# Kernel tuning notes

Hardware: AMD Instinct MI355X
Metric: run time of the kernel (lower is better)

## Reference

```python
import jax, jax.numpy as jnp
import numpy as np
import math

N_HEAD = 32
HEAD_DIM = 64
ROTARY_DIM = 32
ROTARY_BASE = 10000.0
NEG_INF = -10000.0


def _rope_cos_sin(seqlen):
    # RotaryEmbedding._update_cos_sin_cache: inv_freq over even indices of rotary_dim
    inv_freq = 1.0 / (ROTARY_BASE ** (jnp.arange(0, ROTARY_DIM, 2, dtype=jnp.float32) / ROTARY_DIM))
    t = jnp.arange(seqlen, dtype=jnp.float32)
    freqs = jnp.outer(t, inv_freq)  # [s, rd/2]
    return jnp.cos(freqs), jnp.sin(freqs)


def _apply_rotary(t, cos, sin):
    # t: [b, s, h, d]; GPT-NeoX half-rotation on first ROTARY_DIM dims, pass-through rest
    half = ROTARY_DIM // 2
    x1 = t[..., :half]
    x2 = t[..., half:ROTARY_DIM]
    x_pass = t[..., ROTARY_DIM:]
    c = cos[:, None, :]  # [s, 1, rd/2] -> broadcasts over (b, s, h, rd/2)
    s_ = sin[:, None, :]
    return jnp.concatenate([x1 * c - x2 * s_, x1 * s_ + x2 * c, x_pass], axis=-1)


def setup_inputs() -> dict:
    key = jax.random.key(0)
    k1, k2, k3, k4, k5 = jax.random.split(key, 5)
    b, s, e = 2, 2048, 2048
    return {
        "x": jax.random.normal(k1, (b, s, e), dtype=jnp.float32),
        "Wqkv": jax.random.normal(k2, (e, 3 * e), dtype=jnp.float32) * 0.02,
        "bqkv": jax.random.normal(k3, (3 * e,), dtype=jnp.float32) * 0.02,
        "Wout": jax.random.normal(k4, (e, e), dtype=jnp.float32) * 0.02,
        "bout": jax.random.normal(k5, (e,), dtype=jnp.float32) * 0.02,
    }


def reference(x, Wqkv, bqkv, Wout, bout):
    b, s, e = x.shape
    # QKV projection -> [b, s, 3, h, d]
    qkv = (x @ Wqkv + bqkv).reshape(b, s, 3, N_HEAD, HEAD_DIM)
    cos, sin = _rope_cos_sin(s)
    q = _apply_rotary(qkv[:, :, 0], cos, sin)
    k = _apply_rotary(qkv[:, :, 1], cos, sin)
    v = qkv[:, :, 2]
    # Attention (SelfAttention/CrossAttention math, fp32, materialized scores)
    scale = 1.0 / math.sqrt(HEAD_DIM)
    scores = jnp.einsum('bthd,bshd->bhts', q, k * scale)  # [b, h, s, s]
    rows = jnp.arange(s)[:, None]
    cols = jnp.arange(s)[None, :]
    causal_mask = cols > rows  # seqlen_q == seqlen_k
    scores = jnp.where(causal_mask, NEG_INF, scores)
    attn = jax.nn.softmax(scores, axis=-1)
    out = jnp.einsum('bhts,bshd->bthd', attn, v).reshape(b, s, e)
    return out @ Wout + bout
```

## Files before the change

kernel.cpp:

```cpp
#include <hip/hip_runtime.h>


typedef _Float16 half8 __attribute__((ext_vector_type(8)));
typedef _Float16 half4 __attribute__((ext_vector_type(4)));
typedef float floatx4 __attribute__((ext_vector_type(4)));

#define GLD_LDS16(gp, sp)                                        \
  __builtin_amdgcn_global_load_lds(                              \
      (__attribute__((address_space(1))) void*)(gp),             \
      (__attribute__((address_space(3))) void*)(sp), 16, 0, 0)

__device__ __forceinline__ floatx4 mfma16(half8 a, half8 b, floatx4 c) {
  return __builtin_amdgcn_mfma_f32_16x16x32_f16(a, b, c, 0, 0, 0);
}
__device__ __forceinline__ floatx4 mfma16k16(half4 a, half4 b, floatx4 c) {
  return __builtin_amdgcn_mfma_f32_16x16x16f16(a, b, c, 0, 0, 0);
}

__global__ __launch_bounds__(256) void cvt_x_kernel(const float* __restrict__ x,
                                                    _Float16* __restrict__ xh) {
  int idx = blockIdx.x * 256 + threadIdx.x;
  const floatx4* p = (const floatx4*)x + (size_t)idx * 2;
  floatx4 a = p[0], b = p[1];
  half8 o;
#pragma unroll
  for (int j = 0; j < 4; ++j) { o[j] = (_Float16)a[j]; o[4 + j] = (_Float16)b[j]; }
  *((half8*)xh + idx) = o;
}

__global__ __launch_bounds__(256) void cvt_wt_kernel(const float* __restrict__ W,
                                                     _Float16* __restrict__ Wt,
                                                     int Kd, int Nd) {
  __shared__ float tile[64][65];
  int n0 = blockIdx.x * 64, k0 = blockIdx.y * 64;
  int tid = threadIdx.x;
#pragma unroll
  for (int it = 0; it < 4; ++it) {
    int r = (tid >> 4) + it * 16;
    int c = (tid & 15) * 4;
    floatx4 v = *(const floatx4*)(W + (size_t)(k0 + r) * Nd + n0 + c);
    tile[r][c + 0] = v[0]; tile[r][c + 1] = v[1];
    tile[r][c + 2] = v[2]; tile[r][c + 3] = v[3];
  }
  __syncthreads();
#pragma unroll
  for (int it = 0; it < 2; ++it) {
    int r = (tid >> 3) + it * 32;
    int c = (tid & 7) * 8;
    half8 o;
#pragma unroll
    for (int j = 0; j < 8; ++j) o[j] = (_Float16)tile[c + j][r];
    *(half8*)(Wt + (size_t)(n0 + r) * Kd + k0 + c) = o;
  }
}

__global__ __launch_bounds__(512, 2) void gemm_qkv_kernel(
    const _Float16* __restrict__ A, const _Float16* __restrict__ Bt,
    const float* __restrict__ bias,
    _Float16* __restrict__ Qd, _Float16* __restrict__ Kkd,
    _Float16* __restrict__ Vd) {
  __shared__ __align__(16) _Float16 sA[2][16384];
  __shared__ __align__(16) _Float16 sB[2][12288];
  constexpr int KD = 2048;
  constexpr int NT = KD / 64;

  int tid = threadIdx.x, w = tid >> 6, l = tid & 63;
  int lr = l & 15, quad = l >> 4;
  int wr = w >> 1, wc = w & 1;
  int m0 = blockIdx.y * 256, n0 = blockIdx.x * 192;

  int csw0 = ((quad) ^ (lr & 7)) * 8;
  int csw1 = ((quad + 4) ^ (lr & 7)) * 8;

  const _Float16* pA[4];
  const _Float16* pB[3];
  {
    int rl = l >> 3;
    int cs = ((l & 7) ^ rl) * 8;
#pragma unroll
    for (int jj = 0; jj < 4; ++jj)
      pA[jj] = A + (size_t)(m0 + w * 32 + jj * 8 + rl) * KD + cs;
#pragma unroll
    for (int jj = 0; jj < 3; ++jj)
      pB[jj] = Bt + (size_t)(n0 + w * 24 + jj * 8 + rl) * KD + cs;
  }

#define STAGE_ALL(BUF, KT)                                                   \
  _Pragma("unroll") for (int jj = 0; jj < 4; ++jj)                           \
    GLD_LDS16(pA[jj] + (KT), &sA[BUF][(w * 32 + jj * 8) * 64]);              \
  _Pragma("unroll") for (int jj = 0; jj < 3; ++jj)                           \
    GLD_LDS16(pB[jj] + (KT), &sB[BUF][(w * 24 + jj * 8) * 64]);

  floatx4 z4 = {0.f, 0.f, 0.f, 0.f};
  floatx4 acc[4][6];
#pragma unroll
  for (int i = 0; i < 4; ++i)
#pragma unroll
    for (int j = 0; j < 6; ++j) acc[i][j] = z4;

  STAGE_ALL(0, 0);
  asm volatile("s_waitcnt vmcnt(0)" ::: "memory");
  __builtin_amdgcn_s_barrier();

  half8 af[4][2], bf[6][2];
#pragma unroll 2
  for (int t = 0; t < NT; ++t) {
    int buf = t & 1, nbuf = buf ^ 1;
    if (t + 1 < NT) { STAGE_ALL(nbuf, (t + 1) * 64); }
#pragma unroll
    for (int j = 0; j < 6; ++j) {
      int row_ = wc * 96 + j * 16 + lr;
      bf[j][0] = *(const half8*)&sB[buf][row_ * 64 + csw0];
      bf[j][1] = *(const half8*)&sB[buf][row_ * 64 + csw1];
    }
#pragma unroll
    for (int i = 0; i < 4; ++i) {
      int row_ = wr * 64 + i * 16 + lr;
      af[i][0] = *(const half8*)&sA[buf][row_ * 64 + csw0];
      af[i][1] = *(const half8*)&sA[buf][row_ * 64 + csw1];
    }
    __builtin_amdgcn_s_setprio(1);
#pragma unroll
    for (int j = 0; j < 6; ++j)
#pragma unroll
      for (int ks = 0; ks < 2; ++ks)
#pragma unroll
        for (int i = 0; i < 4; ++i)
          acc[i][j] = mfma16(af[i][ks], bf[j][ks], acc[i][j]);
    __builtin_amdgcn_s_setprio(0);
    asm volatile("s_waitcnt vmcnt(0)" ::: "memory");
    __builtin_amdgcn_s_barrier();
  }

  float bj[6];
#pragma unroll
  for (int j = 0; j < 6; ++j) bj[j] = bias[n0 + wc * 96 + j * 16 + lr];
  float freq = __expf(-(float)lr * 0.57564627324851148f);
#pragma unroll
  for (int j = 0; j < 6; ++j) {
    int cb = wc * 96 + j * 16;
    int cg = n0 + cb;
    int which = cg >> 11;
    int d0 = cb & 63;
    int hh = (cg & 2047) >> 6;
    if (which == 2) {
      int dd = d0 + lr;
#pragma unroll
      for (int i = 0; i < 4; ++i) {
        int m = m0 + wr * 64 + i * 16 + quad * 4;
        int bb = m >> 11, tt = m & 2047;
        half4 h;
#pragma unroll
        for (int r = 0; r < 4; ++r) h[r] = (_Float16)(acc[i][j][r] + bj[j]);
        *(half4*)&Vd[(((size_t)(bb * 32 + hh)) * 64 + dd) * 2048 + tt] = h;
      }
    } else if (d0 == 0) {
      _Float16* dst = which ? Kkd : Qd;
#pragma unroll
      for (int i = 0; i < 4; ++i)
#pragma unroll
        for (int r = 0; r < 4; ++r) {
          int m = m0 + wr * 64 + i * 16 + quad * 4 + r;
          int bb = m >> 11, tt = m & 2047;
          float sn, cs2;
          __sincosf((float)tt * freq, &sn, &cs2);
          float x1 = acc[i][j][r] + bj[j];
          float x2 = acc[i][j + 1][r] + bj[j + 1];
          _Float16* row = dst + ((size_t)(bb * 32 + hh) * 2048 + (size_t)tt) * 64;
          row[lr] = (_Float16)(x1 * cs2 - x2 * sn);
          row[lr + 16] = (_Float16)(x1 * sn + x2 * cs2);
        }
    } else if (d0 >= 32) {
      _Float16* dst = which ? Kkd : Qd;
#pragma unroll
      for (int i = 0; i < 4; ++i)
#pragma unroll
        for (int r = 0; r < 4; ++r) {
          int m = m0 + wr * 64 + i * 16 + quad * 4 + r;
          int bb = m >> 11, tt = m & 2047;
          _Float16* row = dst + ((size_t)(bb * 32 + hh) * 2048 + (size_t)tt) * 64;
          row[d0 + lr] = (_Float16)(acc[i][j][r] + bj[j]);
        }
    }
  }
#undef STAGE_ALL
}

__global__ __launch_bounds__(512, 2) void gemm_out_kernel(
    const _Float16* __restrict__ A, const _Float16* __restrict__ Bt,
    const float* __restrict__ bias, float* __restrict__ Co) {
  __shared__ __align__(16) _Float16 sA[2][16384];
  __shared__ __align__(16) _Float16 sB[2][8192];
  constexpr int KD = 2048;
  constexpr int NT = KD / 64;

  int tid = threadIdx.x, w = tid >> 6, l = tid & 63;
  int lr = l & 15, quad = l >> 4;
  int wr = w >> 1, wc = w & 1;
  int m0 = blockIdx.y * 256, n0 = blockIdx.x * 128;

  int csw0 = ((quad) ^ (lr & 7)) * 8;
  int csw1 = ((quad + 4) ^ (lr & 7)) * 8;

  const _Float16* pA[4];
  const _Float16* pB[2];
  {
    int rl = l >> 3;
    int cs = ((l & 7) ^ rl) * 8;
#pragma unroll
    for (int jj = 0; jj < 4; ++jj)
      pA[jj] = A + (size_t)(m0 + w * 32 + jj * 8 + rl) * KD + cs;
#pragma unroll
    for (int jj = 0; jj < 2; ++jj)
      pB[jj] = Bt + (size_t)(n0 + w * 16 + jj * 8 + rl) * KD + cs;
  }

#define STAGE_O(BUF, KT)                                                     \
  _Pragma("unroll") for (int jj = 0; jj < 4; ++jj)                           \
    GLD_LDS16(pA[jj] + (KT), &sA[BUF][(w * 32 + jj * 8) * 64]);              \
  _Pragma("unroll") for (int jj = 0; jj < 2; ++jj)                           \
    GLD_LDS16(pB[jj] + (KT), &sB[BUF][(w * 16 + jj * 8) * 64]);

  floatx4 z4 = {0.f, 0.f, 0.f, 0.f};
  floatx4 acc[4][4];
#pragma unroll
  for (int i = 0; i < 4; ++i)
#pragma unroll
    for (int j = 0; j < 4; ++j) acc[i][j] = z4;

  STAGE_O(0, 0);
  asm volatile("s_waitcnt vmcnt(0)" ::: "memory");
  __builtin_amdgcn_s_barrier();

  half8 af[4][2], bf[4][2];
#pragma unroll 2
  for (int t = 0; t < NT; ++t) {
    int buf = t & 1, nbuf = buf ^ 1;
    if (t + 1 < NT) { STAGE_O(nbuf, (t + 1) * 64); }
#pragma unroll
    for (int j = 0; j < 4; ++j) {
      int row_ = wc * 64 + j * 16 + lr;
      bf[j][0] = *(const half8*)&sB[buf][row_ * 64 + csw0];
      bf[j][1] = *(const half8*)&sB[buf][row_ * 64 + csw1];
    }
#pragma unroll
    for (int i = 0; i < 4; ++i) {
      int row_ = wr * 64 + i * 16 + lr;
      af[i][0] = *(const half8*)&sA[buf][row_ * 64 + csw0];
      af[i][1] = *(const half8*)&sA[buf][row_ * 64 + csw1];
    }
    __builtin_amdgcn_s_setprio(1);
#pragma unroll
    for (int j = 0; j < 4; ++j)
#pragma unroll
      for (int ks = 0; ks < 2; ++ks)
#pragma unroll
        for (int i = 0; i < 4; ++i)
          acc[i][j] = mfma16(af[i][ks], bf[j][ks], acc[i][j]);
    __builtin_amdgcn_s_setprio(0);
    asm volatile("s_waitcnt vmcnt(0)" ::: "memory");
    __builtin_amdgcn_s_barrier();
  }

#pragma unroll
  for (int j = 0; j < 4; ++j) {
    int n = n0 + wc * 64 + j * 16 + lr;
    float bj = bias[n];
#pragma unroll
    for (int i = 0; i < 4; ++i)
#pragma unroll
      for (int r = 0; r < 4; ++r) {
        int m = m0 + wr * 64 + i * 16 + quad * 4 + r;
        Co[(size_t)m * 2048 + n] = acc[i][j][r] + bj;
      }
  }
#undef STAGE_O
}

__global__ __launch_bounds__(256, 4) void attn_kernel(
    const _Float16* __restrict__ Q, const _Float16* __restrict__ Kk,
    const _Float16* __restrict__ Vt, _Float16* __restrict__ O) {
  constexpr int S = 2048;
  int bh = blockIdx.x;
  int qt = 15 - blockIdx.y;
  int bb = bh >> 5, hh = bh & 31;
  const _Float16* Qb = Q + (size_t)bh * S * 64;
  const _Float16* Kb = Kk + (size_t)bh * S * 64;
  const _Float16* Vb = Vt + (size_t)bh * 64 * S;

  __shared__ __align__(16) _Float16 sK[128 * 72];
  __shared__ __align__(16) _Float16 sVt[64 * 136];

  int tid = threadIdx.x, w = tid >> 6, l = tid & 63;
  int lr = l & 15, quad = l >> 4;

  int rk = tid >> 3, ck = (tid & 7) * 8;
  int rv = tid >> 4, cv = (tid & 15) * 8;
  const _Float16* Kst = Kb + (size_t)rk * 64 + ck;
  const _Float16* Vst = Vb + (size_t)rv * S + cv;

  floatx4 z4 = {0.f, 0.f, 0.f, 0.f};
  int q0 = qt * 128;

  half8 qf[2][2];
#pragma unroll
  for (int qtl = 0; qtl < 2; ++qtl)
#pragma unroll
    for (int ks = 0; ks < 2; ++ks) {
      half8 v = *(const half8*)(Qb + (size_t)(q0 + w * 32 + qtl * 16 + lr) * 64 +
                                ks * 32 + quad * 8);
      qf[qtl][ks] = v * (_Float16)0.18033688f;
    }

  floatx4 Oa[4][2];
  float m_i[2] = {-1e30f, -1e30f}, l_i[2] = {0.f, 0.f};
#pragma unroll
  for (int dt = 0; dt < 4; ++dt)
#pragma unroll
    for (int qtl = 0; qtl < 2; ++qtl) Oa[dt][qtl] = z4;

  half8 kpre[4];
#pragma unroll
  for (int it = 0; it < 4; ++it)
    kpre[it] = *(const half8*)(Kst + (size_t)it * 32 * 64);

  for (int jt = 0; jt <= qt; ++jt) {
    half8 vcur[4];
#pragma unroll
    for (int it = 0; it < 4; ++it)
      vcur[it] = *(const half8*)(Vst + (size_t)jt * 128 + (size_t)it * 16 * S);
#pragma unroll
    for (int it = 0; it < 4; ++it)
      *(half8*)&sK[(rk + it * 32) * 72 + ck] = kpre[it];
    if (jt < qt) {
      int kv1 = (jt + 1) * 128;
#pragma unroll
      for (int it = 0; it < 4; ++it)
        kpre[it] = *(const half8*)(Kst + (size_t)(kv1 + it * 32) * 64);
    }
#pragma unroll
    for (int it = 0; it < 4; ++it)
      *(half8*)&sVt[(rv + it * 16) * 136 + cv] = vcur[it];
    __syncthreads();

#pragma unroll
    for (int qtl = 0; qtl < 2; ++qtl) {
      floatx4 Sa[8];
#pragma unroll
      for (int kvt = 0; kvt < 8; ++kvt) Sa[kvt] = z4;
      __builtin_amdgcn_s_setprio(1);
#pragma unroll
      for (int ks = 0; ks < 2; ++ks)
#pragma unroll
        for (int kvt = 0; kvt < 8; ++kvt) {
          half8 kf = *(const half8*)&sK[(kvt * 16 + lr) * 72 + ks * 32 + quad * 8];
          Sa[kvt] = mfma16(kf, qf[qtl][ks], Sa[kvt]);
        }
      __builtin_amdgcn_s_setprio(0);

      if (jt == qt) {
        int q_loc = w * 32 + qtl * 16 + lr;
#pragma unroll
        for (int kvt = 0; kvt < 8; ++kvt) {
          int kv_base = kvt * 16 + quad * 4;
#pragma unroll
          for (int r = 0; r < 4; ++r)
            if (kv_base + r > q_loc) Sa[kvt][r] = -1e30f;
        }
      }

      float mx = Sa[0][0];
#pragma unroll
      for (int kvt = 0; kvt < 8; ++kvt)
#pragma unroll
        for (int r = 0; r < 4; ++r) mx = fmaxf(mx, Sa[kvt][r]);
      mx = fmaxf(mx, __shfl_xor(mx, 16));
      mx = fmaxf(mx, __shfl_xor(mx, 32));
      float mnew = fmaxf(m_i[qtl], mx);
      if (!__all(mx <= m_i[qtl])) {
        float alpha = __builtin_amdgcn_exp2f(m_i[qtl] - mnew);
        l_i[qtl] *= alpha;
#pragma unroll
        for (int dt = 0; dt < 4; ++dt) Oa[dt][qtl] *= alpha;
      }
      m_i[qtl] = mnew;
      float rs = 0.f;
#pragma unroll
      for (int kvt = 0; kvt < 8; ++kvt)
#pragma unroll
        for (int r = 0; r < 4; ++r) {
          float p = __builtin_amdgcn_exp2f(Sa[kvt][r] - mnew);
          Sa[kvt][r] = p;
          rs += p;
        }
      rs += __shfl_xor(rs, 16);
      rs += __shfl_xor(rs, 32);
      l_i[qtl] += rs;

      __builtin_amdgcn_s_setprio(1);
#pragma unroll
      for (int kvt = 0; kvt < 8; ++kvt) {
        half4 vf[4];
#pragma unroll
        for (int dt = 0; dt < 4; ++dt)
          vf[dt] = *(const half4*)&sVt[(dt * 16 + lr) * 136 + kvt * 16 + quad * 4];
        half4 pf;
        pf[0] = (_Float16)Sa[kvt][0];
        pf[1] = (_Float16)Sa[kvt][1];
        pf[2] = (_Float16)Sa[kvt][2];
        pf[3] = (_Float16)Sa[kvt][3];
#pragma unroll
        for (int dt = 0; dt < 4; ++dt)
          Oa[dt][qtl] = mfma16k16(vf[dt], pf, Oa[dt][qtl]);
      }
      __builtin_amdgcn_s_setprio(0);
    }
    __syncthreads();
  }

  float inv0 = 1.0f / l_i[0], inv1 = 1.0f / l_i[1];
#pragma unroll
  for (int dt = 0; dt < 4; ++dt)
#pragma unroll
    for (int qtl = 0; qtl < 2; ++qtl) {
      float inv = qtl ? inv1 : inv0;
      floatx4 o = Oa[dt][qtl];
      half4 hv;
      hv[0] = (_Float16)(o[0] * inv); hv[1] = (_Float16)(o[1] * inv);
      hv[2] = (_Float16)(o[2] * inv); hv[3] = (_Float16)(o[3] * inv);
      *(half4*)&sK[(w * 32 + qtl * 16 + lr) * 72 + dt * 16 + quad * 4] = hv;
    }
  __syncthreads();
#pragma unroll
  for (int it = 0; it < 2; ++it) {
    int row = (tid >> 2) + it * 64;
    int t = q0 + row;
    _Float16* orow = O + ((size_t)(bb * 2048 + t)) * 2048 + hh * 64;
#pragma unroll
    for (int cc = 0; cc < 2; ++cc) {
      int col = (tid & 3) * 16 + cc * 8;
      *(half8*)(orow + col) = *(const half8*)&sK[row * 72 + col];
    }
  }
}

extern "C" void kernel_launch(void* const* d_in, const int* in_sizes, int n_in,
                              void* d_out, int out_size, void* d_ws, size_t ws_size,
                              hipStream_t stream) {
  (void)in_sizes; (void)n_in; (void)out_size; (void)ws_size;
  const float* x = (const float*)d_in[0];
  const float* Wqkv = (const float*)d_in[1];
  const float* bqkv = (const float*)d_in[2];
  const float* Wout = (const float*)d_in[3];
  const float* bout = (const float*)d_in[4];
  float* out = (float*)d_out;
  char* ws = (char*)d_ws;

  _Float16* xh    = (_Float16*)(ws + 0);
  _Float16* wqkvt = (_Float16*)(ws + 16777216);
  _Float16* Oh    = (_Float16*)(ws + 16777216);
  _Float16* Qh    = (_Float16*)(ws + 41943040);
  _Float16* Kh    = (_Float16*)(ws + 58720256);
  _Float16* Vth   = (_Float16*)(ws + 75497472);
  _Float16* woutt = (_Float16*)(ws + 92274688);

  cvt_x_kernel<<<4096, 256, 0, stream>>>(x, xh);
  cvt_wt_kernel<<<dim3(96, 32), 256, 0, stream>>>(Wqkv, wqkvt, 2048, 6144);
  cvt_wt_kernel<<<dim3(32, 32), 256, 0, stream>>>(Wout, woutt, 2048, 2048);
  gemm_qkv_kernel<<<dim3(32, 16), 512, 0, stream>>>(xh, wqkvt, bqkv, Qh, Kh, Vth);
  attn_kernel<<<dim3(64, 16), 256, 0, stream>>>(Qh, Kh, Vth, Oh);
  gemm_out_kernel<<<dim3(16, 16), 512, 0, stream>>>(Oh, woutt, bout, out);
}
```

Measured before the change: 389.8 us.

## Merge conversion kernels, prefetch V tiles, and interleave both query subtiles in attention

Combines the x and weight fp16 conversion kernels into one launch dispatched by block index, removing two kernel launches. In attention, V tiles are now prefetched one iteration ahead into registers, like K, instead of loaded and stored within the same iteration. Both 16-row query subtiles are computed together in the QK and PV MFMA loops, so each K/V fragment read from shared memory feeds two MFMAs. The occupancy hint of 4 blocks is removed from launch_bounds, and together with the extra live registers this may lower occupancy.

Result: no change. 390.8 us (+0.3%).

```diff
diff --git a/kernel.cpp b/kernel.cpp
--- a/kernel.cpp
+++ b/kernel.cpp
@@ -17,23 +17,34 @@
   return __builtin_amdgcn_mfma_f32_16x16x16f16(a, b, c, 0, 0, 0);
 }
 
-__global__ __launch_bounds__(256) void cvt_x_kernel(const float* __restrict__ x,
-                                                    _Float16* __restrict__ xh) {
-  int idx = blockIdx.x * 256 + threadIdx.x;
-  const floatx4* p = (const floatx4*)x + (size_t)idx * 2;
-  floatx4 a = p[0], b = p[1];
-  half8 o;
-#pragma unroll
-  for (int j = 0; j < 4; ++j) { o[j] = (_Float16)a[j]; o[4 + j] = (_Float16)b[j]; }
-  *((half8*)xh + idx) = o;
-}
-
-__global__ __launch_bounds__(256) void cvt_wt_kernel(const float* __restrict__ W,
-                                                     _Float16* __restrict__ Wt,
-                                                     int Kd, int Nd) {
+__global__ __launch_bounds__(256) void cvt_all_kernel(
+    const float* __restrict__ x, _Float16* __restrict__ xh,
+    const float* __restrict__ Wqkv, _Float16* __restrict__ wqkvt,
+    const float* __restrict__ Wout, _Float16* __restrict__ woutt) {
   __shared__ float tile[64][65];
-  int n0 = blockIdx.x * 64, k0 = blockIdx.y * 64;
-  int tid = threadIdx.x;
+  int b = blockIdx.x, tid = threadIdx.x;
+  if (b < 4096) {
+    int idx = b * 256 + tid;
+    const floatx4* p = (const floatx4*)x + (size_t)idx * 2;
+    floatx4 a = p[0], b2 = p[1];
+    half8 o;
+#pragma unroll
+    for (int j = 0; j < 4; ++j) { o[j] = (_Float16)a[j]; o[4 + j] = (_Float16)b2[j]; }
+    *((half8*)xh + idx) = o;
+    return;
+  }
+  const float* W;
+  _Float16* Wt;
+  int Kd, Nd, n0, k0;
+  if (b < 7168) {
+    int bb = b - 4096;
+    W = Wqkv; Wt = wqkvt; Kd = 2048; Nd = 6144;
+    n0 = (bb % 96) * 64; k0 = (bb / 96) * 64;
+  } else {
+    int bb = b - 7168;
+    W = Wout; Wt = woutt; Kd = 2048; Nd = 2048;
+    n0 = (bb % 32) * 64; k0 = (bb / 32) * 64;
+  }
 #pragma unroll
   for (int it = 0; it < 4; ++it) {
     int r = (tid >> 4) + it * 16;
@@ -277,7 +288,7 @@
 #undef STAGE_O
 }
 
-__global__ __launch_bounds__(256, 4) void attn_kernel(
+__global__ __launch_bounds__(256) void attn_kernel(
     const _Float16* __restrict__ Q, const _Float16* __restrict__ Kk,
     const _Float16* __restrict__ Vt, _Float16* __restrict__ O) {
   constexpr int S = 2048;
@@ -319,61 +330,67 @@
 #pragma unroll
     for (int qtl = 0; qtl < 2; ++qtl) Oa[dt][qtl] = z4;
 
-  half8 kpre[4];
-#pragma unroll
-  for (int it = 0; it < 4; ++it)
+  half8 kpre[4], vpre[4];
+#pragma unroll
+  for (int it = 0; it < 4; ++it) {
     kpre[it] = *(const half8*)(Kst + (size_t)it * 32 * 64);
+    vpre[it] = *(const half8*)(Vst + (size_t)it * 16 * S);
+  }
 
   for (int jt = 0; jt <= qt; ++jt) {
-    half8 vcur[4];
-#pragma unroll
-    for (int it = 0; it < 4; ++it)
-      vcur[it] = *(const half8*)(Vst + (size_t)jt * 128 + (size_t)it * 16 * S);
-#pragma unroll
-    for (int it = 0; it < 4; ++it)
+#pragma unroll
+    for (int it = 0; it < 4; ++it) {
       *(half8*)&sK[(rk + it * 32) * 72 + ck] = kpre[it];
+      *(half8*)&sVt[(rv + it * 16) * 136 + cv] = vpre[it];
+    }
     if (jt < qt) {
       int kv1 = (jt + 1) * 128;
 #pragma unroll
-      for (int it = 0; it < 4; ++it)
+      for (int it = 0; it < 4; ++it) {
         kpre[it] = *(const half8*)(Kst + (size_t)(kv1 + it * 32) * 64);
-    }
-#pragma unroll
-    for (int it = 0; it < 4; ++it)
-      *(half8*)&sVt[(rv + it * 16) * 136 + cv] = vcur[it];
+        vpre[it] = *(const half8*)(Vst + kv1 + (size_t)it * 16 * S);
+      }
+    }
     __syncthreads();
 
-#pragma unroll
-    for (int qtl = 0; qtl < 2; ++qtl) {
-      floatx4 Sa[8];
-#pragma unroll
-      for (int kvt = 0; kvt < 8; ++kvt) Sa[kvt] = z4;
-      __builtin_amdgcn_s_setprio(1);
-#pragma unroll
-      for (int ks = 0; ks < 2; ++ks)
-#pragma unroll
-        for (int kvt = 0; kvt < 8; ++kvt) {
-          half8 kf = *(const half8*)&sK[(kvt * 16 + lr) * 72 + ks * 32 + quad * 8];
-          Sa[kvt] = mfma16(kf, qf[qtl][ks], Sa[kvt]);
-        }
-      __builtin_amdgcn_s_setprio(0);
-
-      if (jt == qt) {
+    floatx4 Sa[2][8];
+#pragma unroll
+    for (int qtl = 0; qtl < 2; ++qtl)
+#pragma unroll
+      for (int kvt = 0; kvt < 8; ++kvt) Sa[qtl][kvt] = z4;
+    __builtin_amdgcn_s_setprio(1);
+#pragma unroll
+    for (int ks = 0; ks < 2; ++ks) {
+#pragma unroll
+      for (int kvt = 0; kvt < 8; ++kvt) {
+        half8 kf = *(const half8*)&sK[(kvt * 16 + lr) * 72 + ks * 32 + quad * 8];
+        Sa[0][kvt] = mfma16(kf, qf[0][ks], Sa[0][kvt]);
+        Sa[1][kvt] = mfma16(kf, qf[1][ks], Sa[1][kvt]);
+      }
+    }
+    __builtin_amdgcn_s_setprio(0);
+
+    if (jt == qt) {
+#pragma unroll
+      for (int qtl = 0; qtl < 2; ++qtl) {
         int q_loc = w * 32 + qtl * 16 + lr;
 #pragma unroll
         for (int kvt = 0; kvt < 8; ++kvt) {
           int kv_base = kvt * 16 + quad * 4;
 #pragma unroll
           for (int r = 0; r < 4; ++r)
-            if (kv_base + r > q_loc) Sa[kvt][r] = -1e30f;
+            if (kv_base + r > q_loc) Sa[qtl][kvt][r] = -1e30f;
         }
       }
-
-      float mx = Sa[0][0];
+    }
+
+#pragma unroll
+    for (int qtl = 0; qtl < 2; ++qtl) {
+      float mx = Sa[qtl][0][0];
 #pragma unroll
       for (int kvt = 0; kvt < 8; ++kvt)
 #pragma unroll
-        for (int r = 0; r < 4; ++r) mx = fmaxf(mx, Sa[kvt][r]);
+        for (int r = 0; r < 4; ++r) mx = fmaxf(mx, Sa[qtl][kvt][r]);
       mx = fmaxf(mx, __shfl_xor(mx, 16));
       mx = fmaxf(mx, __shfl_xor(mx, 32));
       float mnew = fmaxf(m_i[qtl], mx);
@@ -389,32 +406,37 @@
       for (int kvt = 0; kvt < 8; ++kvt)
 #pragma unroll
         for (int r = 0; r < 4; ++r) {
-          float p = __builtin_amdgcn_exp2f(Sa[kvt][r] - mnew);
-          Sa[kvt][r] = p;
+          float p = __builtin_amdgcn_exp2f(Sa[qtl][kvt][r] - mnew);
+          Sa[qtl][kvt][r] = p;
           rs += p;
         }
       rs += __shfl_xor(rs, 16);
       rs += __shfl_xor(rs, 32);
       l_i[qtl] += rs;
-
-      __builtin_amdgcn_s_setprio(1);
-#pragma unroll
-      for (int kvt = 0; kvt < 8; ++kvt) {
-        half4 vf[4];
-#pragma unroll
-        for (int dt = 0; dt < 4; ++dt)
-          vf[dt] = *(const half4*)&sVt[(dt * 16 + lr) * 136 + kvt * 16 + quad * 4];
-        half4 pf;
-        pf[0] = (_Float16)Sa[kvt][0];
-        pf[1] = (_Float16)Sa[kvt][1];
-        pf[2] = (_Float16)Sa[kvt][2];
-        pf[3] = (_Float16)Sa[kvt][3];
-#pragma unroll
-        for (int dt = 0; dt < 4; ++dt)
-          Oa[dt][qtl] = mfma16k16(vf[dt], pf, Oa[dt][qtl]);
-      }
-      __builtin_amdgcn_s_setprio(0);
-    }
+    }
+
+    __builtin_amdgcn_s_setprio(1);
+#pragma unroll
+    for (int kvt = 0; kvt < 8; ++kvt) {
+      half4 vf[4];
+#pragma unroll
+      for (int dt = 0; dt < 4; ++dt)
+        vf[dt] = *(const half4*)&sVt[(dt * 16 + lr) * 136 + kvt * 16 + quad * 4];
+      half4 pf[2];
+#pragma unroll
+      for (int qtl = 0; qtl < 2; ++qtl) {
+        pf[qtl][0] = (_Float16)Sa[qtl][kvt][0];
+        pf[qtl][1] = (_Float16)Sa[qtl][kvt][1];
+        pf[qtl][2] = (_Float16)Sa[qtl][kvt][2];
+        pf[qtl][3] = (_Float16)Sa[qtl][kvt][3];
+      }
+#pragma unroll
+      for (int dt = 0; dt < 4; ++dt)
+#pragma unroll
+        for (int qtl = 0; qtl < 2; ++qtl)
+          Oa[dt][qtl] = mfma16k16(vf[dt], pf[qtl], Oa[dt][qtl]);
+    }
+    __builtin_amdgcn_s_setprio(0);
     __syncthreads();
   }
 
@@ -464,9 +486,7 @@
   _Float16* Vth   = (_Float16*)(ws + 75497472);
   _Float16* woutt = (_Float16*)(ws + 92274688);
 
-  cvt_x_kernel<<<4096, 256, 0, stream>>>(x, xh);
-  cvt_wt_kernel<<<dim3(96, 32), 256, 0, stream>>>(Wqkv, wqkvt, 2048, 6144);
-  cvt_wt_kernel<<<dim3(32, 32), 256, 0, stream>>>(Wout, woutt, 2048, 2048);
+  cvt_all_kernel<<<8192, 256, 0, stream>>>(x, xh, Wqkv, wqkvt, Wout, woutt);
   gemm_qkv_kernel<<<dim3(32, 16), 512, 0, stream>>>(xh, wqkvt, bqkv, Qh, Kh, Vth);
   attn_kernel<<<dim3(64, 16), 256, 0, stream>>>(Qh, Kh, Vth, Oh);
   gemm_out_kernel<<<dim3(16, 16), 512, 0, stream>>>(Oh, woutt, bout, out);
```
